# Performance work log

Measured on AMD Instinct MI355X. Metric: run time of the kernel, lower is better.

The kernel has to match this reference:

```python
import jax, jax.numpy as jnp
import numpy as np

C = 256
CQK = C // 8  # 32


def setup_inputs() -> dict:
    key = jax.random.key(0)
    ks = jax.random.split(key, 8)
    B, H, W = 4, 64, 64
    x = jax.random.normal(ks[0], (B, H, W, C), dtype=jnp.float32)
    # 1x1 conv weights == dense projections over channel dim
    Wf = jax.random.normal(ks[1], (C, CQK), dtype=jnp.float32) * (1.0 / np.sqrt(C))
    bf = jnp.zeros((CQK,), dtype=jnp.float32)
    Wg = jax.random.normal(ks[2], (C, CQK), dtype=jnp.float32) * (1.0 / np.sqrt(C))
    bg = jnp.zeros((CQK,), dtype=jnp.float32)
    Wh = jax.random.normal(ks[3], (C, C), dtype=jnp.float32) * (1.0 / np.sqrt(C))
    bh = jnp.zeros((C,), dtype=jnp.float32)
    gamma = jnp.float32(0.5)  # nonzero so attention path contributes
    return {"x": x, "Wf": Wf, "bf": bf, "Wg": Wg, "bg": bg, "Wh": Wh, "bh": bh, "gamma": gamma}


def reference(x, Wf, bf, Wg, bg, Wh, bh, gamma):
    B, H, W, Cc = x.shape
    N = H * W
    xf = x.reshape(B, N, Cc)                       # hw_flatten
    f = xf @ Wf + bf                               # [B, N, C//8] keys
    g = xf @ Wg + bg                               # [B, N, C//8] queries
    h = xf @ Wh + bh                               # [B, N, C] values
    s = jnp.einsum('bnc,bmc->bnm', g, f)           # [B, N, N]
    b = jax.nn.softmax(s, axis=-1)
    o = jnp.einsum('bnm,bmc->bnc', b, h)           # [B, N, C]
    y = gamma * o.reshape(B, H, W, Cc) + x
    return y
```

## Files before the change

kernel.cpp:

```cpp
#include <hip/hip_runtime.h>
#include <hip/hip_bf16.h>

#define BATCH 4
#define NSEQ  4096
#define CDIM  256
#define CQK   32
#define L2E   1.44269504088896340736f

typedef short bf16x8 __attribute__((ext_vector_type(8)));
typedef float f32x16 __attribute__((ext_vector_type(16)));
typedef unsigned short u16;
typedef unsigned int   u32;
typedef unsigned int   u32x4 __attribute__((ext_vector_type(4)));

__device__ __forceinline__ u32 pk2(float lo, float hi) {
  u16 a = __builtin_bit_cast(u16, __float2bfloat16(lo));
  u16 b = __builtin_bit_cast(u16, __float2bfloat16(hi));
  return (u32)a | ((u32)b << 16);
}
__device__ __forceinline__ bf16x8 ld8(const u16* p) {
  uint4 u = *(const uint4*)p;
  return __builtin_bit_cast(bf16x8, u);
}
__device__ __forceinline__ float exp2_raw(float x) {
#if __has_builtin(__builtin_amdgcn_exp2f)
  return __builtin_amdgcn_exp2f(x);
#else
  return exp2f(x);
#endif
}

__global__ __launch_bounds__(64) void prep_kernel(
    const float* __restrict__ Wf, const float* __restrict__ Wg, const float* __restrict__ Wh,
    u16* __restrict__ wfT, u16* __restrict__ wgT, u16* __restrict__ whT) {
  const int cb = blockIdx.x, t = threadIdx.x;
#pragma unroll
  for (int j = 0; j < 4; ++j) {
    const int k = t + j * 64;
    if (cb < 32) {
      wfT[cb * 256 + k] = (u16)(pk2(Wf[k * CQK + cb] * L2E, 0.f) & 0xFFFF);
    } else if (cb < 64) {
      const int c = cb - 32;
      wgT[c * 256 + k] = (u16)(pk2(Wg[k * CQK + c], 0.f) & 0xFFFF);
    } else {
      const int c = cb - 64;
      whT[c * 256 + k] = (u16)(pk2(Wh[k * CDIM + c], 0.f) & 0xFFFF);
    }
  }
}

__global__ __launch_bounds__(256, 1) void proj_kernel(
    const float* __restrict__ x,
    const float* __restrict__ bfv, const float* __restrict__ bgv, const float* __restrict__ bhv,
    const u16* __restrict__ wfT, const u16* __restrict__ wgT, const u16* __restrict__ whT,
    u16* __restrict__ fP, u16* __restrict__ g_ws, u16* __restrict__ hP) {
  const int tid   = threadIdx.x;
  const int lan   = tid & 63;
  const int lan31 = lan & 31;
  const int g2    = lan >> 5;
  const int w     = tid >> 6;
  const int half  = w >> 1;
  const int row0  = blockIdx.x * 64 + (w & 1) * 32;
  const int b     = row0 >> 12;
  const int kcg   = row0 >> 5;

  bf16x8 xf[16];
  const float* xr = x + ((size_t)row0 + lan31) * CDIM + g2 * 8;
#pragma unroll
  for (int ks = 0; ks < 16; ++ks) {
    float4 a = *(const float4*)(xr + ks * 16);
    float4 c = *(const float4*)(xr + ks * 16 + 4);
    u32x4 u = { pk2(a.x, a.y), pk2(a.z, a.w), pk2(c.x, c.y), pk2(c.z, c.w) };
    xf[ks] = __builtin_bit_cast(bf16x8, u);
  }

  {
    const u16*  wT   = half ? wgT : wfT;
    const float bias = half ? bgv[lan31] : bfv[lan31] * L2E;
    f32x16 acc;
#pragma unroll
    for (int r = 0; r < 16; ++r) acc[r] = bias;
    const u16* wp = wT + lan31 * 256 + g2 * 8;
#pragma unroll
    for (int ks = 0; ks < 16; ++ks)
      acc = __builtin_amdgcn_mfma_f32_32x32x16_bf16(xf[ks], ld8(wp + ks * 16), acc, 0, 0, 0);
    if (half) {
#pragma unroll
      for (int r = 0; r < 16; ++r) {
        const int row = (r & 3) + 8 * (r >> 2) + 4 * g2;
        g_ws[((size_t)row0 + row) * CQK + lan31] = (u16)(pk2(acc[r], 0.f) & 0xFFFF);
      }
    } else {
      u16* fb = fP + (size_t)kcg * 1024
              + (lan31 >> 4) * 512 + ((lan31 >> 3) & 1) * 256 + (lan31 & 7);
#pragma unroll
      for (int r = 0; r < 16; ++r) {
        const int crow = (r & 3) + 8 * (r >> 2) + 4 * g2;
        fb[crow * 8] = (u16)(pk2(acc[r], 0.f) & 0xFFFF);
      }
    }
  }

#pragma unroll
  for (int t = 0; t < 4; ++t) {
    const int ct = half * 128 + t * 32;
    f32x16 acc;
#pragma unroll
    for (int r = 0; r < 16; ++r)
      acc[r] = bhv[ct + (r & 3) + 8 * (r >> 2) + 4 * g2];
    const u16* wp = whT + (size_t)(ct + lan31) * 256 + g2 * 8;
#pragma unroll
    for (int ks = 0; ks < 16; ++ks)
      acc = __builtin_amdgcn_mfma_f32_32x32x16_bf16(ld8(wp + ks * 16), xf[ks], acc, 0, 0, 0);
    const int cg = half * 4 + t;
    u16* hb = hP + ((size_t)(b * 8 + cg) * 128 + ((row0 & (NSEQ - 1)) >> 5)) * 1024
            + (lan31 >> 4) * 512 + ((lan31 >> 3) & 1) * 256 + (lan31 & 7);
#pragma unroll
    for (int r = 0; r < 16; ++r) {
      const int crow = (r & 3) + 8 * (r >> 2) + 4 * g2;
      hb[crow * 8] = (u16)(pk2(acc[r], 0.f) & 0xFFFF);
    }
  }
}

__global__ __launch_bounds__(512, 2) void attn_kernel(
    const float* __restrict__ x, const float* __restrict__ gamma_p,
    const u16* __restrict__ fP, const u16* __restrict__ g_ws,
    const u16* __restrict__ hP, float* __restrict__ out) {
  __shared__ u32x4 xb[2][4][4][2][64];
  __shared__ u32   pls[4][2][2][16][64];
  __shared__ float lsh[4][4][64];

  const int tid   = threadIdx.x;
  const int lan   = tid & 63;
  const int lan31 = lan & 31;
  const int g2    = lan >> 5;
  const int w     = tid >> 6;
  const int kw    = w & 3;
  const int cq    = w >> 2;
  const int bid   = blockIdx.x;
  const int xcd   = bid & 7;
  const int b     = xcd >> 1;
  const int inner = bid >> 3;
  const int cb    = inner & 1;
  const int n0    = (((xcd & 1) << 4) | (inner >> 1)) * 128;

  const float gamma = gamma_p[0];

  bf16x8 bgM[2][2];
#pragma unroll
  for (int qhl = 0; qhl < 2; ++qhl) {
    const u16* gp = g_ws + ((size_t)b * NSEQ + n0 + (cq * 2 + qhl) * 32 + lan31) * CQK + g2 * 8;
    bgM[qhl][0] = ld8(gp);
    bgM[qhl][1] = ld8(gp + 16);
  }

  f32x16 o[2][4], zfrag;
#pragma unroll
  for (int r = 0; r < 16; ++r) zfrag[r] = 0.f;
#pragma unroll
  for (int cg = 0; cg < 2; ++cg)
#pragma unroll
    for (int qh = 0; qh < 4; ++qh) o[cg][qh] = zfrag;
  float l2[2] = {0.f, 0.f};

  const u16* fpk  = fP + (size_t)(b * 128 + kw * 32) * 1024 + lan * 8;
  const u16* hpk0 = hP + ((size_t)(b * 8 + cb * 4 + cq * 2) * 128 + kw * 32) * 1024 + lan * 8;
  const u16* hpk1 = hpk0 + (size_t)128 * 1024;

  bf16x8 af0 = ld8(fpk), af1 = ld8(fpk + 512);
  fpk += 1024;

  for (int it = 0; it < 32; ++it) {
    const int p = it & 1;
    bf16x8 naf0 = ld8(fpk), naf1 = ld8(fpk + 512);
    fpk += 1024;
    bf16x8 ha0 = ld8(hpk0), hb0 = ld8(hpk0 + 512);
    bf16x8 ha1 = ld8(hpk1), hb1 = ld8(hpk1 + 512);
    hpk0 += 1024; hpk1 += 1024;

#pragma unroll
    for (int qhl = 0; qhl < 2; ++qhl) {
      f32x16 s = __builtin_amdgcn_mfma_f32_32x32x16_bf16(af0, bgM[qhl][0], zfrag, 0, 0, 0);
      s        = __builtin_amdgcn_mfma_f32_32x32x16_bf16(af1, bgM[qhl][1], s,     0, 0, 0);

      float pv[16];
#pragma unroll
      for (int r = 0; r < 16; ++r) pv[r] = exp2_raw(s[r]);
      float rs = ((pv[0]+pv[1])+(pv[2]+pv[3])) + ((pv[4]+pv[5])+(pv[6]+pv[7]))
               + ((pv[8]+pv[9])+(pv[10]+pv[11])) + ((pv[12]+pv[13])+(pv[14]+pv[15]));
      auto rr = __builtin_amdgcn_permlane32_swap(__builtin_bit_cast(u32, rs),
                                                 __builtin_bit_cast(u32, rs), false, false);
      l2[qhl] += __builtin_bit_cast(float, (u32)rr[0]) + __builtin_bit_cast(float, (u32)rr[1]);

      u32 q0a = pk2(pv[0],pv[1]),   q0b = pk2(pv[2],pv[3]);
      u32 q1a = pk2(pv[4],pv[5]),   q1b = pk2(pv[6],pv[7]);
      u32 q2a = pk2(pv[8],pv[9]),   q2b = pk2(pv[10],pv[11]);
      u32 q3a = pk2(pv[12],pv[13]), q3b = pk2(pv[14],pv[15]);
      auto r02a = __builtin_amdgcn_permlane32_swap(q0a, q1a, false, false);
      auto r13a = __builtin_amdgcn_permlane32_swap(q0b, q1b, false, false);
      auto r02b = __builtin_amdgcn_permlane32_swap(q2a, q3a, false, false);
      auto r13b = __builtin_amdgcn_permlane32_swap(q2b, q3b, false, false);
      u32x4 u0 = {(u32)r02a[0], (u32)r13a[0], (u32)r02a[1], (u32)r13a[1]};
      u32x4 u1 = {(u32)r02b[0], (u32)r13b[0], (u32)r02b[1], (u32)r13b[1]};
      xb[p][kw][cq * 2 + qhl][0][lan] = u0;
      xb[p][kw][cq * 2 + qhl][1][lan] = u1;
    }

    __syncthreads();

    bf16x8 ap[4][2];
#pragma unroll
    for (int qh = 0; qh < 4; ++qh) {
      ap[qh][0] = __builtin_bit_cast(bf16x8, xb[p][kw][qh][0][lan]);
      ap[qh][1] = __builtin_bit_cast(bf16x8, xb[p][kw][qh][1][lan]);
    }

#pragma unroll
    for (int qh = 0; qh < 4; ++qh) {
      o[0][qh] = __builtin_amdgcn_mfma_f32_32x32x16_bf16(ap[qh][0], ha0, o[0][qh], 0, 0, 0);
      o[0][qh] = __builtin_amdgcn_mfma_f32_32x32x16_bf16(ap[qh][1], hb0, o[0][qh], 0, 0, 0);
      o[1][qh] = __builtin_amdgcn_mfma_f32_32x32x16_bf16(ap[qh][0], ha1, o[1][qh], 0, 0, 0);
      o[1][qh] = __builtin_amdgcn_mfma_f32_32x32x16_bf16(ap[qh][1], hb1, o[1][qh], 0, 0, 0);
    }

    af0 = naf0; af1 = naf1;
  }

  lsh[kw][cq * 2 + 0][lan] = l2[0];
  lsh[kw][cq * 2 + 1][lan] = l2[1];

#pragma unroll
  for (int round = 0; round < 2; ++round) {
    __syncthreads();
    {
#pragma unroll
      for (int qhl = 0; qhl < 2; ++qhl)
#pragma unroll
        for (int r = 0; r < 16; ++r)
          pls[kw][cq][qhl][r][lan] = pk2(o[0][round * 2 + qhl][r], o[1][round * 2 + qhl][r]);
    }
    __syncthreads();
    {
      const int qhl = kw & 1, rb = (kw >> 1) * 8;
      const int qh  = round * 2 + qhl;
      float e0[8], e1[8];
#pragma unroll
      for (int j = 0; j < 8; ++j) { e0[j] = 0.f; e1[j] = 0.f; }
#pragma unroll
      for (int kk = 0; kk < 4; ++kk)
#pragma unroll
        for (int j = 0; j < 8; ++j) {
          u32 v = pls[kk][cq][qhl][rb + j][lan];
          e0[j] += __builtin_bit_cast(float, v << 16);
          e1[j] += __builtin_bit_cast(float, v & 0xFFFF0000u);
        }
      const float l_tot = lsh[0][qh][lan] + lsh[1][qh][lan]
                        + lsh[2][qh][lan] + lsh[3][qh][lan];
      const float gi = gamma / l_tot;
#pragma unroll
      for (int j = 0; j < 8; ++j) {
        const int r  = rb + j;
        const int nl = (r & 3) + 8 * (r >> 2) + 4 * g2;
        const float gir = __shfl(gi, nl);
        const size_t row = (size_t)b * NSEQ + n0 + qh * 32 + nl;
        const size_t i0 = row * CDIM + cb * 128 + cq * 64 + lan31;
        out[i0]      = fmaf(gir, e0[j], x[i0]);
        out[i0 + 32] = fmaf(gir, e1[j], x[i0 + 32]);
      }
    }
  }
}

extern "C" void kernel_launch(void* const* d_in, const int* in_sizes, int n_in,
                              void* d_out, int out_size, void* d_ws, size_t ws_size,
                              hipStream_t stream) {
  const float* x     = (const float*)d_in[0];
  const float* Wf    = (const float*)d_in[1];
  const float* bf    = (const float*)d_in[2];
  const float* Wg    = (const float*)d_in[3];
  const float* bg    = (const float*)d_in[4];
  const float* Wh    = (const float*)d_in[5];
  const float* bh    = (const float*)d_in[6];
  const float* gamma = (const float*)d_in[7];
  float* out = (float*)d_out;

  u16* hP   = (u16*)d_ws;
  u16* fPp  = hP  + (size_t)BATCH * CDIM * NSEQ;
  u16* g_ws = fPp + (size_t)BATCH * NSEQ * CQK;
  u16* wfT  = g_ws + (size_t)BATCH * NSEQ * CQK;
  u16* wgT  = wfT + (size_t)CQK * CDIM;
  u16* whT  = wgT + (size_t)CQK * CDIM;

  hipLaunchKernelGGL(prep_kernel, dim3(320), dim3(64), 0, stream,
                     Wf, Wg, Wh, wfT, wgT, whT);
  hipLaunchKernelGGL(proj_kernel, dim3(256), dim3(256), 0, stream,
                     x, bf, bg, bh, wfT, wgT, whT, fPp, g_ws, hP);
  hipLaunchKernelGGL(attn_kernel, dim3(256), dim3(512), 0, stream,
                     x, gamma, fPp, g_ws, hP, out);
}
```

Measured before the change: 82.30 us.

## Restructure attention to 64-query blocks with rotating-wave softmax and MFMA row sums

The attention kernel now processes 64 queries per block, with 512 blocks instead of 256. Its 8 waves split as 2 query halves by 4 channel groups, and each wave accumulates its output over all keys directly, which removes the cross-wave key-split reduction through shared memory in the epilogue. Softmax tiles are computed by one wave per step in rotation and shared through a three-slot LDS buffer. Row sums are produced by an MFMA against a ones vector instead of scalar adds plus permlane swaps. In exchange, every one of the 128 key chunks needs a block-wide barrier, and the exp work runs on only one wave per step, which risks serialization stalls.

```diff
diff --git a/kernel.cpp b/kernel.cpp
--- a/kernel.cpp
+++ b/kernel.cpp
@@ -123,152 +123,111 @@
   }
 }
 
-__global__ __launch_bounds__(512, 2) void attn_kernel(
+__global__ __launch_bounds__(512, 4) void attn_kernel(
     const float* __restrict__ x, const float* __restrict__ gamma_p,
     const u16* __restrict__ fP, const u16* __restrict__ g_ws,
     const u16* __restrict__ hP, float* __restrict__ out) {
-  __shared__ u32x4 xb[2][4][4][2][64];
-  __shared__ u32   pls[4][2][2][16][64];
-  __shared__ float lsh[4][4][64];
+  __shared__ u32x4 xb[3][2][2][64];
+  __shared__ float lsh[2][32];
 
   const int tid   = threadIdx.x;
   const int lan   = tid & 63;
   const int lan31 = lan & 31;
   const int g2    = lan >> 5;
   const int w     = tid >> 6;
-  const int kw    = w & 3;
-  const int cq    = w >> 2;
+  const int qh    = w >> 2;
+  const int cgl   = w & 3;
   const int bid   = blockIdx.x;
   const int xcd   = bid & 7;
   const int b     = xcd >> 1;
   const int inner = bid >> 3;
   const int cb    = inner & 1;
-  const int n0    = (((xcd & 1) << 4) | (inner >> 1)) * 128;
+  const int n0    = ((((xcd & 1) << 5) | (inner >> 1))) * 64;
 
   const float gamma = gamma_p[0];
 
-  bf16x8 bgM[2][2];
-#pragma unroll
-  for (int qhl = 0; qhl < 2; ++qhl) {
-    const u16* gp = g_ws + ((size_t)b * NSEQ + n0 + (cq * 2 + qhl) * 32 + lan31) * CQK + g2 * 8;
-    bgM[qhl][0] = ld8(gp);
-    bgM[qhl][1] = ld8(gp + 16);
-  }
-
-  f32x16 o[2][4], zfrag;
+  const u16* gp = g_ws + ((size_t)b * NSEQ + n0 + qh * 32 + lan31) * CQK + g2 * 8;
+  bf16x8 bg0 = ld8(gp), bg1 = ld8(gp + 16);
+
+  const u32x4 onesu = {0x3F803F80u, 0x3F803F80u, 0x3F803F80u, 0x3F803F80u};
+  const bf16x8 ones = __builtin_bit_cast(bf16x8, onesu);
+
+  f32x16 o, lacc, zfrag;
 #pragma unroll
   for (int r = 0; r < 16; ++r) zfrag[r] = 0.f;
-#pragma unroll
-  for (int cg = 0; cg < 2; ++cg)
-#pragma unroll
-    for (int qh = 0; qh < 4; ++qh) o[cg][qh] = zfrag;
-  float l2[2] = {0.f, 0.f};
-
-  const u16* fpk  = fP + (size_t)(b * 128 + kw * 32) * 1024 + lan * 8;
-  const u16* hpk0 = hP + ((size_t)(b * 8 + cb * 4 + cq * 2) * 128 + kw * 32) * 1024 + lan * 8;
-  const u16* hpk1 = hpk0 + (size_t)128 * 1024;
-
-  bf16x8 af0 = ld8(fpk), af1 = ld8(fpk + 512);
-  fpk += 1024;
-
-  for (int it = 0; it < 32; ++it) {
-    const int p = it & 1;
-    bf16x8 naf0 = ld8(fpk), naf1 = ld8(fpk + 512);
-    fpk += 1024;
-    bf16x8 ha0 = ld8(hpk0), hb0 = ld8(hpk0 + 512);
-    bf16x8 ha1 = ld8(hpk1), hb1 = ld8(hpk1 + 512);
-    hpk0 += 1024; hpk1 += 1024;
-
-#pragma unroll
-    for (int qhl = 0; qhl < 2; ++qhl) {
-      f32x16 s = __builtin_amdgcn_mfma_f32_32x32x16_bf16(af0, bgM[qhl][0], zfrag, 0, 0, 0);
-      s        = __builtin_amdgcn_mfma_f32_32x32x16_bf16(af1, bgM[qhl][1], s,     0, 0, 0);
-
-      float pv[16];
-#pragma unroll
-      for (int r = 0; r < 16; ++r) pv[r] = exp2_raw(s[r]);
-      float rs = ((pv[0]+pv[1])+(pv[2]+pv[3])) + ((pv[4]+pv[5])+(pv[6]+pv[7]))
-               + ((pv[8]+pv[9])+(pv[10]+pv[11])) + ((pv[12]+pv[13])+(pv[14]+pv[15]));
-      auto rr = __builtin_amdgcn_permlane32_swap(__builtin_bit_cast(u32, rs),
-                                                 __builtin_bit_cast(u32, rs), false, false);
-      l2[qhl] += __builtin_bit_cast(float, (u32)rr[0]) + __builtin_bit_cast(float, (u32)rr[1]);
-
-      u32 q0a = pk2(pv[0],pv[1]),   q0b = pk2(pv[2],pv[3]);
-      u32 q1a = pk2(pv[4],pv[5]),   q1b = pk2(pv[6],pv[7]);
-      u32 q2a = pk2(pv[8],pv[9]),   q2b = pk2(pv[10],pv[11]);
-      u32 q3a = pk2(pv[12],pv[13]), q3b = pk2(pv[14],pv[15]);
-      auto r02a = __builtin_amdgcn_permlane32_swap(q0a, q1a, false, false);
-      auto r13a = __builtin_amdgcn_permlane32_swap(q0b, q1b, false, false);
-      auto r02b = __builtin_amdgcn_permlane32_swap(q2a, q3a, false, false);
-      auto r13b = __builtin_amdgcn_permlane32_swap(q2b, q3b, false, false);
-      u32x4 u0 = {(u32)r02a[0], (u32)r13a[0], (u32)r02a[1], (u32)r13a[1]};
-      u32x4 u1 = {(u32)r02b[0], (u32)r13b[0], (u32)r02b[1], (u32)r13b[1]};
-      xb[p][kw][cq * 2 + qhl][0][lan] = u0;
-      xb[p][kw][cq * 2 + qhl][1][lan] = u1;
-    }
-
+  o = zfrag; lacc = zfrag;
+
+  const u16* fbase = fP + (size_t)b * 128 * 1024 + lan * 8;
+  const u16* hpk   = hP + (size_t)(b * 8 + cb * 4 + cgl) * 128 * 1024 + lan * 8;
+
+  bf16x8 mf0 = ld8(fbase + (size_t)cgl * 1024);
+  bf16x8 mf1 = ld8(fbase + (size_t)cgl * 1024 + 512);
+
+  auto sm_pack = [&](int slot) {
+    f32x16 s = __builtin_amdgcn_mfma_f32_32x32x16_bf16(mf0, bg0, zfrag, 0, 0, 0);
+    s        = __builtin_amdgcn_mfma_f32_32x32x16_bf16(mf1, bg1, s,     0, 0, 0);
+    float pv[16];
+#pragma unroll
+    for (int r = 0; r < 16; ++r) pv[r] = exp2_raw(s[r]);
+    u32 q0a = pk2(pv[0],pv[1]),   q0b = pk2(pv[2],pv[3]);
+    u32 q1a = pk2(pv[4],pv[5]),   q1b = pk2(pv[6],pv[7]);
+    u32 q2a = pk2(pv[8],pv[9]),   q2b = pk2(pv[10],pv[11]);
+    u32 q3a = pk2(pv[12],pv[13]), q3b = pk2(pv[14],pv[15]);
+    auto r02a = __builtin_amdgcn_permlane32_swap(q0a, q1a, false, false);
+    auto r13a = __builtin_amdgcn_permlane32_swap(q0b, q1b, false, false);
+    auto r02b = __builtin_amdgcn_permlane32_swap(q2a, q3a, false, false);
+    auto r13b = __builtin_amdgcn_permlane32_swap(q2b, q3b, false, false);
+    u32x4 u0 = {(u32)r02a[0], (u32)r13a[0], (u32)r02a[1], (u32)r13a[1]};
+    u32x4 u1 = {(u32)r02b[0], (u32)r13b[0], (u32)r02b[1], (u32)r13b[1]};
+    xb[slot][qh][0][lan] = u0;
+    xb[slot][qh][1][lan] = u1;
+  };
+
+  if (cgl == 0) {
+    sm_pack(0);
+    mf0 = ld8(fbase + 4 * 1024);
+    mf1 = ld8(fbase + 4 * 1024 + 512);
+  }
+  __syncthreads();
+
+  bf16x8 ha = ld8(hpk), hb = ld8(hpk + 512);
+  hpk += 1024;
+
+  for (int c = 0; c < 128; ++c) {
+    if (cgl == ((c + 1) & 3) && c + 1 < 128) {
+      sm_pack((c + 1) % 3);
+      mf0 = ld8(fbase + (size_t)(c + 5) * 1024);
+      mf1 = ld8(fbase + (size_t)(c + 5) * 1024 + 512);
+    }
     __syncthreads();
-
-    bf16x8 ap[4][2];
-#pragma unroll
-    for (int qh = 0; qh < 4; ++qh) {
-      ap[qh][0] = __builtin_bit_cast(bf16x8, xb[p][kw][qh][0][lan]);
-      ap[qh][1] = __builtin_bit_cast(bf16x8, xb[p][kw][qh][1][lan]);
-    }
-
-#pragma unroll
-    for (int qh = 0; qh < 4; ++qh) {
-      o[0][qh] = __builtin_amdgcn_mfma_f32_32x32x16_bf16(ap[qh][0], ha0, o[0][qh], 0, 0, 0);
-      o[0][qh] = __builtin_amdgcn_mfma_f32_32x32x16_bf16(ap[qh][1], hb0, o[0][qh], 0, 0, 0);
-      o[1][qh] = __builtin_amdgcn_mfma_f32_32x32x16_bf16(ap[qh][0], ha1, o[1][qh], 0, 0, 0);
-      o[1][qh] = __builtin_amdgcn_mfma_f32_32x32x16_bf16(ap[qh][1], hb1, o[1][qh], 0, 0, 0);
-    }
-
-    af0 = naf0; af1 = naf1;
-  }
-
-  lsh[kw][cq * 2 + 0][lan] = l2[0];
-  lsh[kw][cq * 2 + 1][lan] = l2[1];
-
-#pragma unroll
-  for (int round = 0; round < 2; ++round) {
-    __syncthreads();
-    {
-#pragma unroll
-      for (int qhl = 0; qhl < 2; ++qhl)
-#pragma unroll
-        for (int r = 0; r < 16; ++r)
-          pls[kw][cq][qhl][r][lan] = pk2(o[0][round * 2 + qhl][r], o[1][round * 2 + qhl][r]);
-    }
-    __syncthreads();
-    {
-      const int qhl = kw & 1, rb = (kw >> 1) * 8;
-      const int qh  = round * 2 + qhl;
-      float e0[8], e1[8];
-#pragma unroll
-      for (int j = 0; j < 8; ++j) { e0[j] = 0.f; e1[j] = 0.f; }
-#pragma unroll
-      for (int kk = 0; kk < 4; ++kk)
-#pragma unroll
-        for (int j = 0; j < 8; ++j) {
-          u32 v = pls[kk][cq][qhl][rb + j][lan];
-          e0[j] += __builtin_bit_cast(float, v << 16);
-          e1[j] += __builtin_bit_cast(float, v & 0xFFFF0000u);
-        }
-      const float l_tot = lsh[0][qh][lan] + lsh[1][qh][lan]
-                        + lsh[2][qh][lan] + lsh[3][qh][lan];
-      const float gi = gamma / l_tot;
-#pragma unroll
-      for (int j = 0; j < 8; ++j) {
-        const int r  = rb + j;
-        const int nl = (r & 3) + 8 * (r >> 2) + 4 * g2;
-        const float gir = __shfl(gi, nl);
-        const size_t row = (size_t)b * NSEQ + n0 + qh * 32 + nl;
-        const size_t i0 = row * CDIM + cb * 128 + cq * 64 + lan31;
-        out[i0]      = fmaf(gir, e0[j], x[i0]);
-        out[i0 + 32] = fmaf(gir, e1[j], x[i0 + 32]);
-      }
-    }
+    bf16x8 ap0 = __builtin_bit_cast(bf16x8, xb[c % 3][qh][0][lan]);
+    bf16x8 ap1 = __builtin_bit_cast(bf16x8, xb[c % 3][qh][1][lan]);
+    o = __builtin_amdgcn_mfma_f32_32x32x16_bf16(ap0, ha, o, 0, 0, 0);
+    o = __builtin_amdgcn_mfma_f32_32x32x16_bf16(ap1, hb, o, 0, 0, 0);
+    if (cgl == 3) {
+      lacc = __builtin_amdgcn_mfma_f32_32x32x16_bf16(ap0, ones, lacc, 0, 0, 0);
+      lacc = __builtin_amdgcn_mfma_f32_32x32x16_bf16(ap1, ones, lacc, 0, 0, 0);
+    }
+    ha = ld8(hpk); hb = ld8(hpk + 512);
+    hpk += 1024;
+  }
+
+  if (cgl == 3 && lan31 == 0) {
+#pragma unroll
+    for (int r = 0; r < 16; ++r) {
+      const int row = (r & 3) + 8 * (r >> 2) + 4 * g2;
+      lsh[qh][row] = lacc[r];
+    }
+  }
+  __syncthreads();
+
+  const size_t orow = (size_t)b * NSEQ + n0 + qh * 32;
+#pragma unroll
+  for (int r = 0; r < 16; ++r) {
+    const int row = (r & 3) + 8 * (r >> 2) + 4 * g2;
+    const float gi = gamma / lsh[qh][row];
+    const size_t i0 = (orow + row) * CDIM + cb * 128 + cgl * 32 + lan31;
+    out[i0] = fmaf(gi, o[r], x[i0]);
   }
 }
 
@@ -296,6 +255,6 @@
                      Wf, Wg, Wh, wfT, wgT, whT);
   hipLaunchKernelGGL(proj_kernel, dim3(256), dim3(256), 0, stream,
                      x, bf, bg, bh, wfT, wgT, whT, fPp, g_ws, hP);
-  hipLaunchKernelGGL(attn_kernel, dim3(256), dim3(512), 0, stream,
+  hipLaunchKernelGGL(attn_kernel, dim3(512), dim3(512), 0, stream,
                      x, gamma, fPp, g_ws, hP, out);
 }
```

Result: slower. 115.2 us (+39.9%).

## Split attention work so each wave computes all value channels without LDS exchange

Applied to the files above, without the earlier changes.

The attention kernel now uses 256-thread blocks over 64-query tiles with 512 blocks. Each wave computes its own probability tile and immediately feeds it to PV MFMAs for all four channel groups. This removes the per-iteration shared-memory exchange of probabilities and the __syncthreads inside the main loop. The cost is that each wave loads four times more value data per iteration and holds more accumulator registers. The number of blocks that must recompute QK scores also doubles.

```diff
diff --git a/kernel.cpp b/kernel.cpp
--- a/kernel.cpp
+++ b/kernel.cpp
@@ -123,66 +123,64 @@
   }
 }
 
-__global__ __launch_bounds__(512, 2) void attn_kernel(
+__global__ __launch_bounds__(256, 2) void attn_kernel(
     const float* __restrict__ x, const float* __restrict__ gamma_p,
     const u16* __restrict__ fP, const u16* __restrict__ g_ws,
     const u16* __restrict__ hP, float* __restrict__ out) {
-  __shared__ u32x4 xb[2][4][4][2][64];
   __shared__ u32   pls[4][2][2][16][64];
-  __shared__ float lsh[4][4][64];
+  __shared__ float lsh[4][2][64];
 
   const int tid   = threadIdx.x;
   const int lan   = tid & 63;
   const int lan31 = lan & 31;
   const int g2    = lan >> 5;
-  const int w     = tid >> 6;
-  const int kw    = w & 3;
-  const int cq    = w >> 2;
+  const int kw    = tid >> 6;
   const int bid   = blockIdx.x;
   const int xcd   = bid & 7;
   const int b     = xcd >> 1;
   const int inner = bid >> 3;
   const int cb    = inner & 1;
-  const int n0    = (((xcd & 1) << 4) | (inner >> 1)) * 128;
+  const int n0    = ((((xcd & 1) << 5) | (inner >> 1))) * 64;
 
   const float gamma = gamma_p[0];
 
   bf16x8 bgM[2][2];
 #pragma unroll
-  for (int qhl = 0; qhl < 2; ++qhl) {
-    const u16* gp = g_ws + ((size_t)b * NSEQ + n0 + (cq * 2 + qhl) * 32 + lan31) * CQK + g2 * 8;
-    bgM[qhl][0] = ld8(gp);
-    bgM[qhl][1] = ld8(gp + 16);
-  }
-
-  f32x16 o[2][4], zfrag;
+  for (int qh = 0; qh < 2; ++qh) {
+    const u16* gp = g_ws + ((size_t)b * NSEQ + n0 + qh * 32 + lan31) * CQK + g2 * 8;
+    bgM[qh][0] = ld8(gp);
+    bgM[qh][1] = ld8(gp + 16);
+  }
+
+  f32x16 o[4][2], zfrag;
 #pragma unroll
   for (int r = 0; r < 16; ++r) zfrag[r] = 0.f;
 #pragma unroll
-  for (int cg = 0; cg < 2; ++cg)
-#pragma unroll
-    for (int qh = 0; qh < 4; ++qh) o[cg][qh] = zfrag;
+  for (int cg = 0; cg < 4; ++cg) { o[cg][0] = zfrag; o[cg][1] = zfrag; }
   float l2[2] = {0.f, 0.f};
 
-  const u16* fpk  = fP + (size_t)(b * 128 + kw * 32) * 1024 + lan * 8;
-  const u16* hpk0 = hP + ((size_t)(b * 8 + cb * 4 + cq * 2) * 128 + kw * 32) * 1024 + lan * 8;
-  const u16* hpk1 = hpk0 + (size_t)128 * 1024;
+  const u16*  fpk = fP + (size_t)(b * 128 + kw * 32) * 1024 + lan * 8;
+  const u16*  hpk = hP + ((size_t)(b * 8 + cb * 4) * 128 + kw * 32) * 1024 + lan * 8;
+  const size_t hcg = (size_t)128 * 1024;
 
   bf16x8 af0 = ld8(fpk), af1 = ld8(fpk + 512);
   fpk += 1024;
 
   for (int it = 0; it < 32; ++it) {
-    const int p = it & 1;
     bf16x8 naf0 = ld8(fpk), naf1 = ld8(fpk + 512);
     fpk += 1024;
-    bf16x8 ha0 = ld8(hpk0), hb0 = ld8(hpk0 + 512);
-    bf16x8 ha1 = ld8(hpk1), hb1 = ld8(hpk1 + 512);
-    hpk0 += 1024; hpk1 += 1024;
-
-#pragma unroll
-    for (int qhl = 0; qhl < 2; ++qhl) {
-      f32x16 s = __builtin_amdgcn_mfma_f32_32x32x16_bf16(af0, bgM[qhl][0], zfrag, 0, 0, 0);
-      s        = __builtin_amdgcn_mfma_f32_32x32x16_bf16(af1, bgM[qhl][1], s,     0, 0, 0);
+    bf16x8 ha[4], hb[4];
+#pragma unroll
+    for (int cg = 0; cg < 4; ++cg) {
+      ha[cg] = ld8(hpk + cg * hcg);
+      hb[cg] = ld8(hpk + cg * hcg + 512);
+    }
+    hpk += 1024;
+
+#pragma unroll
+    for (int qh = 0; qh < 2; ++qh) {
+      f32x16 s = __builtin_amdgcn_mfma_f32_32x32x16_bf16(af0, bgM[qh][0], zfrag, 0, 0, 0);
+      s        = __builtin_amdgcn_mfma_f32_32x32x16_bf16(af1, bgM[qh][1], s,     0, 0, 0);
 
       float pv[16];
 #pragma unroll
@@ -191,7 +189,7 @@
                + ((pv[8]+pv[9])+(pv[10]+pv[11])) + ((pv[12]+pv[13])+(pv[14]+pv[15]));
       auto rr = __builtin_amdgcn_permlane32_swap(__builtin_bit_cast(u32, rs),
                                                  __builtin_bit_cast(u32, rs), false, false);
-      l2[qhl] += __builtin_bit_cast(float, (u32)rr[0]) + __builtin_bit_cast(float, (u32)rr[1]);
+      l2[qh] += __builtin_bit_cast(float, (u32)rr[0]) + __builtin_bit_cast(float, (u32)rr[1]);
 
       u32 q0a = pk2(pv[0],pv[1]),   q0b = pk2(pv[2],pv[3]);
       u32 q1a = pk2(pv[4],pv[5]),   q1b = pk2(pv[6],pv[7]);
@@ -203,72 +201,53 @@
       auto r13b = __builtin_amdgcn_permlane32_swap(q2b, q3b, false, false);
       u32x4 u0 = {(u32)r02a[0], (u32)r13a[0], (u32)r02a[1], (u32)r13a[1]};
       u32x4 u1 = {(u32)r02b[0], (u32)r13b[0], (u32)r02b[1], (u32)r13b[1]};
-      xb[p][kw][cq * 2 + qhl][0][lan] = u0;
-      xb[p][kw][cq * 2 + qhl][1][lan] = u1;
-    }
-
-    __syncthreads();
-
-    bf16x8 ap[4][2];
-#pragma unroll
-    for (int qh = 0; qh < 4; ++qh) {
-      ap[qh][0] = __builtin_bit_cast(bf16x8, xb[p][kw][qh][0][lan]);
-      ap[qh][1] = __builtin_bit_cast(bf16x8, xb[p][kw][qh][1][lan]);
-    }
-
-#pragma unroll
-    for (int qh = 0; qh < 4; ++qh) {
-      o[0][qh] = __builtin_amdgcn_mfma_f32_32x32x16_bf16(ap[qh][0], ha0, o[0][qh], 0, 0, 0);
-      o[0][qh] = __builtin_amdgcn_mfma_f32_32x32x16_bf16(ap[qh][1], hb0, o[0][qh], 0, 0, 0);
-      o[1][qh] = __builtin_amdgcn_mfma_f32_32x32x16_bf16(ap[qh][0], ha1, o[1][qh], 0, 0, 0);
-      o[1][qh] = __builtin_amdgcn_mfma_f32_32x32x16_bf16(ap[qh][1], hb1, o[1][qh], 0, 0, 0);
+      bf16x8 ap0 = __builtin_bit_cast(bf16x8, u0);
+      bf16x8 ap1 = __builtin_bit_cast(bf16x8, u1);
+
+#pragma unroll
+      for (int cg = 0; cg < 4; ++cg) {
+        o[cg][qh] = __builtin_amdgcn_mfma_f32_32x32x16_bf16(ap0, ha[cg], o[cg][qh], 0, 0, 0);
+        o[cg][qh] = __builtin_amdgcn_mfma_f32_32x32x16_bf16(ap1, hb[cg], o[cg][qh], 0, 0, 0);
+      }
     }
 
     af0 = naf0; af1 = naf1;
   }
 
-  lsh[kw][cq * 2 + 0][lan] = l2[0];
-  lsh[kw][cq * 2 + 1][lan] = l2[1];
-
-#pragma unroll
-  for (int round = 0; round < 2; ++round) {
-    __syncthreads();
-    {
-#pragma unroll
-      for (int qhl = 0; qhl < 2; ++qhl)
-#pragma unroll
-        for (int r = 0; r < 16; ++r)
-          pls[kw][cq][qhl][r][lan] = pk2(o[0][round * 2 + qhl][r], o[1][round * 2 + qhl][r]);
-    }
-    __syncthreads();
-    {
-      const int qhl = kw & 1, rb = (kw >> 1) * 8;
-      const int qh  = round * 2 + qhl;
-      float e0[8], e1[8];
-#pragma unroll
-      for (int j = 0; j < 8; ++j) { e0[j] = 0.f; e1[j] = 0.f; }
-#pragma unroll
-      for (int kk = 0; kk < 4; ++kk)
-#pragma unroll
-        for (int j = 0; j < 8; ++j) {
-          u32 v = pls[kk][cq][qhl][rb + j][lan];
-          e0[j] += __builtin_bit_cast(float, v << 16);
-          e1[j] += __builtin_bit_cast(float, v & 0xFFFF0000u);
-        }
-      const float l_tot = lsh[0][qh][lan] + lsh[1][qh][lan]
-                        + lsh[2][qh][lan] + lsh[3][qh][lan];
-      const float gi = gamma / l_tot;
-#pragma unroll
-      for (int j = 0; j < 8; ++j) {
-        const int r  = rb + j;
-        const int nl = (r & 3) + 8 * (r >> 2) + 4 * g2;
-        const float gir = __shfl(gi, nl);
-        const size_t row = (size_t)b * NSEQ + n0 + qh * 32 + nl;
-        const size_t i0 = row * CDIM + cb * 128 + cq * 64 + lan31;
-        out[i0]      = fmaf(gir, e0[j], x[i0]);
-        out[i0 + 32] = fmaf(gir, e1[j], x[i0 + 32]);
-      }
-    }
+  lsh[kw][0][lan] = l2[0];
+  lsh[kw][1][lan] = l2[1];
+#pragma unroll
+  for (int cgp = 0; cgp < 2; ++cgp)
+#pragma unroll
+    for (int qh = 0; qh < 2; ++qh)
+#pragma unroll
+      for (int r = 0; r < 16; ++r)
+        pls[kw][cgp][qh][r][lan] = pk2(o[cgp * 2][qh][r], o[cgp * 2 + 1][qh][r]);
+  __syncthreads();
+
+  const int cgp = kw >> 1, qh = kw & 1;
+  float e0[16], e1[16];
+#pragma unroll
+  for (int r = 0; r < 16; ++r) { e0[r] = 0.f; e1[r] = 0.f; }
+#pragma unroll
+  for (int kk = 0; kk < 4; ++kk)
+#pragma unroll
+    for (int r = 0; r < 16; ++r) {
+      u32 v = pls[kk][cgp][qh][r][lan];
+      e0[r] += __builtin_bit_cast(float, v << 16);
+      e1[r] += __builtin_bit_cast(float, v & 0xFFFF0000u);
+    }
+  const float l_tot = lsh[0][qh][lan] + lsh[1][qh][lan]
+                    + lsh[2][qh][lan] + lsh[3][qh][lan];
+  const float gi = gamma / l_tot;
+#pragma unroll
+  for (int r = 0; r < 16; ++r) {
+    const int nl = (r & 3) + 8 * (r >> 2) + 4 * g2;
+    const float gir = __shfl(gi, nl);
+    const size_t row = (size_t)b * NSEQ + n0 + qh * 32 + nl;
+    const size_t i0 = row * CDIM + cb * 128 + cgp * 64 + lan31;
+    out[i0]      = fmaf(gir, e0[r], x[i0]);
+    out[i0 + 32] = fmaf(gir, e1[r], x[i0 + 32]);
   }
 }
 
@@ -296,6 +275,6 @@
                      Wf, Wg, Wh, wfT, wgT, whT);
   hipLaunchKernelGGL(proj_kernel, dim3(256), dim3(256), 0, stream,
                      x, bf, bg, bh, wfT, wgT, whT, fPp, g_ws, hP);
-  hipLaunchKernelGGL(attn_kernel, dim3(256), dim3(512), 0, stream,
+  hipLaunchKernelGGL(attn_kernel, dim3(512), dim3(256), 0, stream,
                      x, gamma, fPp, g_ws, hP, out);
 }
```

Result: faster. 80.55 us (-2.1%).
